# Kernel optimization log

Hardware: AMD Instinct MI355X
Metric: run time of the kernel (lower is better)

The kernel has to match this reference:

```python
import jax, jax.numpy as jnp
import numpy as np

BS, SLEN = 4, 4096
H, ZD, VD = 8, 128, 256
CHUNK = 1024
NEG = -1e9


def _rope(x, cos, sin):
    # x: [B, S, H, D]; cos/sin: [S, D//2] (llama-style complex pair rotation)
    b, s, h, d = x.shape
    xr, xi = x.reshape(b, s, h, d // 2, 2)[..., 0], x.reshape(b, s, h, d // 2, 2)[..., 1]
    c = cos[None, :, None, :]
    sn = sin[None, :, None, :]
    orr = xr * c - xi * sn
    oii = xr * sn + xi * c
    return jnp.stack([orr, oii], axis=-1).reshape(b, s, h, d)


def setup_inputs() -> dict:
    key = jax.random.key(0)
    k1, k2, k3 = jax.random.split(key, 3)
    xq = jax.random.normal(k1, (BS, SLEN, H * ZD), dtype=jnp.float32)
    xk = jax.random.normal(k2, (BS, SLEN, H * ZD), dtype=jnp.float32)
    xv = jax.random.normal(k3, (BS, SLEN, H * VD), dtype=jnp.float32)
    # rotary tables over one chunk
    freqs = 1.0 / (10000.0 ** (np.arange(0, ZD, 2, dtype=np.float32) / ZD))  # [ZD//2]
    t = np.arange(CHUNK, dtype=np.float32)
    ang = np.outer(t, freqs)  # [CHUNK, ZD//2]
    cos = jnp.asarray(np.cos(ang), dtype=jnp.float32)
    sin = jnp.asarray(np.sin(ang), dtype=jnp.float32)
    # additive causal mask within a chunk
    causal = np.tril(np.ones((CHUNK, CHUNK), dtype=bool))
    mask = jnp.asarray(np.where(causal, 0.0, NEG).astype(np.float32))
    return {"xq": xq, "xk": xk, "xv": xv, "mask": mask, "cos": cos, "sin": sin}


def reference(xq, xk, xv, mask, cos, sin):
    bs, slen, _ = xq.shape
    nc = slen // CHUNK
    q = xq.reshape(bs * nc, CHUNK, H, ZD)
    k = xk.reshape(bs * nc, CHUNK, H, ZD)
    v = xv.reshape(bs * nc, CHUNK, H, VD)
    # RoPE applied after chunking (slen > chunk_size path)
    q = _rope(q, cos, sin)
    k = _rope(k, cos, sin)
    # block-local causal attention, no 1/sqrt(d) scaling (faithful to source)
    scores = jnp.einsum("bqhd,bkhd->bhqk", q, k) + mask[None, None, :, :]
    probs = jax.nn.softmax(scores.astype(jnp.float32), axis=-1).astype(q.dtype)
    out = jnp.einsum("bhqk,bkhd->bqhd", probs, v)
    return out.reshape(bs, slen, H * VD)
```

## Files before the change

### kernel.cpp

```cpp
#include <hip/hip_runtime.h>


#define NHEAD 8
#define ZDIM  128
#define VDIM  256
#define CHUNK 1024
#define QTILE 128
#define KT    32
#define NW    4

typedef _Float16 f16x8 __attribute__((ext_vector_type(8)));
typedef _Float16 f16x4 __attribute__((ext_vector_type(4)));
typedef __fp16   h16x2 __attribute__((ext_vector_type(2)));
typedef float    f32x4 __attribute__((ext_vector_type(4)));
typedef unsigned int u32;

#define KSTRIDE 136
#define VSTRIDE 40
#define PSTRIDE 76
#define LOG2E   1.44269504088896f
#define RTHR    11.5415603f

__global__ __launch_bounds__(256, 2)
void attn_fused(const float* __restrict__ xq, const float* __restrict__ xk,
                const float* __restrict__ xv, const float* __restrict__ cosT,
                const float* __restrict__ sinT, float* __restrict__ out)
{
  __shared__ _Float16 Klds[2][KT * KSTRIDE];
  __shared__ _Float16 Vlds[2][VDIM * VSTRIDE];
  __shared__ _Float16 Plds[NW * 32 * PSTRIDE];

  const int b = (int)blockIdx.x;
  const int d = (b & 7) * 64 + (b >> 3);
  const int qpair = d & 3;
  const int ch = d >> 2;
  const int h  = ch & 7;
  const int cb = ch >> 3;

  const int tid  = threadIdx.x;
  const int w    = tid >> 6;
  const int lane = tid & 63;
  const int l15  = lane & 15;
  const int lhi  = lane >> 4;

  const size_t row0 = (size_t)cb * CHUNK;

  const int kr   = tid >> 3;
  const int kc0  = (tid & 7) * 16;
  const int vg   = tid >> 5;
  const int vc0  = (tid & 31) * 8;
  const int vsw  = tid & 3;
  const int kblk = vg >> 1;
  const int inb  = (vg & 1) * 4;

  int buf = 0;

  for (int half = 0; half < 2; ++half) {
    const int qt = half ? qpair : (7 - qpair);

    f16x8 qfrag[2][4];
#pragma unroll
    for (int s = 0; s < 2; ++s) {
      const int qrow = qt * QTILE + w * 32 + s * 16 + l15;
      const float* qp = xq + (row0 + qrow) * (size_t)(NHEAD * ZDIM) + h * ZDIM;
      const float* cq = cosT + qrow * (ZDIM / 2);
      const float* sq = sinT + qrow * (ZDIM / 2);
#pragma unroll
      for (int blk = 0; blk < 4; ++blk) {
        const int d0 = blk * 32 + lhi * 8;
        f32x4 a  = *(const f32x4*)(qp + d0);
        f32x4 bb = *(const f32x4*)(qp + d0 + 4);
        union { h16x2 h2[4]; f16x8 v; } fr;
#pragma unroll
        for (int p = 0; p < 4; ++p) {
          const float cv = cq[(d0 >> 1) + p];
          const float sv = sq[(d0 >> 1) + p];
          const float xr = (p < 2 ? a[2 * p] : bb[2 * p - 4]);
          const float xi = (p < 2 ? a[2 * p + 1] : bb[2 * p - 3]);
          fr.h2[p] = __builtin_amdgcn_cvt_pkrtz(xr * cv - xi * sv, xr * sv + xi * cv);
        }
        qfrag[s][blk] = fr.v;
      }
    }

    const f32x4 zf = {0.f, 0.f, 0.f, 0.f};
    f32x4 acc[2][16];
#pragma unroll
    for (int s = 0; s < 2; ++s)
#pragma unroll
      for (int i = 0; i < 16; ++i) acc[s][i] = zf;
    float mrun2[2][4], lrun[2][4];
#pragma unroll
    for (int s = 0; s < 2; ++s)
#pragma unroll
      for (int r = 0; r < 4; ++r) { mrun2[s][r] = -1e30f; lrun[s][r] = 0.f; }

    const int nkt = 4 * (qt + 1);
    const int wq0 = qt * QTILE + w * 32;

    for (int kt = 0; kt < nkt; ++kt) {
      const int ktb = kt * KT;
      {
        const int krow = ktb + kr;
        const float* kp = xk + (row0 + krow) * (size_t)(NHEAD * ZDIM) + h * ZDIM + kc0;
        const float* ck = cosT + krow * (ZDIM / 2) + (kc0 >> 1);
        const float* sk = sinT + krow * (ZDIM / 2) + (kc0 >> 1);
        f32x4 k0 = *(const f32x4*)(kp);      f32x4 k1 = *(const f32x4*)(kp + 4);
        f32x4 k2 = *(const f32x4*)(kp + 8);  f32x4 k3 = *(const f32x4*)(kp + 12);
        f32x4 c0 = *(const f32x4*)(ck);      f32x4 c1 = *(const f32x4*)(ck + 4);
        f32x4 s0 = *(const f32x4*)(sk);      f32x4 s1 = *(const f32x4*)(sk + 4);
        union { h16x2 h2[8]; u32 u[8]; } ko;
#pragma unroll
        for (int p = 0; p < 8; ++p) {
          const float cv = (p < 4 ? c0[p] : c1[p - 4]);
          const float sv = (p < 4 ? s0[p] : s1[p - 4]);
          const int j = 2 * p;
          const float xr = (j < 4 ? k0[j] : j < 8 ? k1[j - 4] : j < 12 ? k2[j - 8] : k3[j - 12]);
          const float xi = (j + 1 < 4 ? k0[j + 1] : j + 1 < 8 ? k1[j - 3] : j + 1 < 12 ? k2[j - 7] : k3[j - 11]);
          ko.h2[p] = __builtin_amdgcn_cvt_pkrtz(xr * cv - xi * sv, xr * sv + xi * cv);
        }
        u32* kdst = (u32*)&Klds[buf][kr * KSTRIDE + kc0];
        kdst[0] = ko.u[0]; kdst[1] = ko.u[1]; kdst[2] = ko.u[2]; kdst[3] = ko.u[3];
        kdst[4] = ko.u[4]; kdst[5] = ko.u[5]; kdst[6] = ko.u[6]; kdst[7] = ko.u[7];
      }
      {
        const int vrow = ktb + vg * 4;
        const float* vp = xv + (row0 + vrow) * (size_t)(NHEAD * VDIM) + h * VDIM + vc0;
        f32x4 v0 = *(const f32x4*)(vp);         f32x4 v1 = *(const f32x4*)(vp + 4);
        f32x4 v2 = *(const f32x4*)(vp + 2048);  f32x4 v3 = *(const f32x4*)(vp + 2052);
        f32x4 v4 = *(const f32x4*)(vp + 4096);  f32x4 v5 = *(const f32x4*)(vp + 4100);
        f32x4 v6 = *(const f32x4*)(vp + 6144);  f32x4 v7 = *(const f32x4*)(vp + 6148);
#pragma unroll
        for (int ci = 0; ci < 8; ++ci) {
          const float e0 = (ci < 4 ? v0[ci] : v1[ci - 4]);
          const float e1 = (ci < 4 ? v2[ci] : v3[ci - 4]);
          const float e2 = (ci < 4 ? v4[ci] : v5[ci - 4]);
          const float e3 = (ci < 4 ? v6[ci] : v7[ci - 4]);
          union { h16x2 a[2]; f16x4 v; } t;
          t.a[0] = __builtin_amdgcn_cvt_pkrtz(e0, e1);
          t.a[1] = __builtin_amdgcn_cvt_pkrtz(e2, e3);
          *(f16x4*)&Vlds[buf][(vc0 + ci) * VSTRIDE + ((kblk ^ vsw) * 8) + inb] = t.v;
        }
      }
      __syncthreads();

      if (ktb <= wq0 + 31) {
        f32x4 sf[2][2];
#pragma unroll
        for (int s = 0; s < 2; ++s)
#pragma unroll
          for (int n = 0; n < 2; ++n) sf[s][n] = zf;
#pragma unroll
        for (int n = 0; n < 2; ++n) {
#pragma unroll
          for (int blk = 0; blk < 4; ++blk) {
            f16x8 bfr = *(const f16x8*)&Klds[buf][(n * 16 + l15) * KSTRIDE + blk * 32 + lhi * 8];
            sf[0][n] = __builtin_amdgcn_mfma_f32_16x16x32_f16(qfrag[0][blk], bfr, sf[0][n], 0, 0, 0);
            sf[1][n] = __builtin_amdgcn_mfma_f32_16x16x32_f16(qfrag[1][blk], bfr, sf[1][n], 0, 0, 0);
          }
        }

        if (ktb + 31 > wq0) {
#pragma unroll
          for (int s = 0; s < 2; ++s) {
            const int qg = wq0 + s * 16 + lhi * 4;
#pragma unroll
            for (int n = 0; n < 2; ++n) {
              const int kg = ktb + n * 16 + l15;
#pragma unroll
              for (int r = 0; r < 4; ++r)
                if (kg > qg + r) sf[s][n][r] = -1.0e9f;
            }
          }
        }

        float mx2v[2][4];
        bool need = false;
#pragma unroll
        for (int s = 0; s < 2; ++s) {
#pragma unroll
          for (int r = 0; r < 4; ++r) {
            float mx = fmaxf(sf[s][0][r], sf[s][1][r]);
            mx = fmaxf(mx, __shfl_xor(mx, 1));
            mx = fmaxf(mx, __shfl_xor(mx, 2));
            mx = fmaxf(mx, __shfl_xor(mx, 4));
            mx = fmaxf(mx, __shfl_xor(mx, 8));
            mx2v[s][r] = mx * LOG2E;
            need = need || (mx2v[s][r] > mrun2[s][r] + RTHR);
          }
        }
        if (__any(need)) {
#pragma unroll
          for (int s = 0; s < 2; ++s) {
#pragma unroll
            for (int r = 0; r < 4; ++r) {
              const float Mn2 = fmaxf(mrun2[s][r], mx2v[s][r]);
              const float al = exp2f(mrun2[s][r] - Mn2);
              mrun2[s][r] = Mn2;
              lrun[s][r] *= al;
#pragma unroll
              for (int i = 0; i < 16; ++i) acc[s][i][r] *= al;
            }
          }
        }
#pragma unroll
        for (int s = 0; s < 2; ++s) {
#pragma unroll
          for (int r = 0; r < 4; ++r) {
#pragma unroll
            for (int n = 0; n < 2; ++n) {
              const float p = exp2f(fmaf(sf[s][n][r], LOG2E, -mrun2[s][r]));
              lrun[s][r] += p;
              Plds[(w * 32 + s * 16 + lhi * 4 + r) * PSTRIDE + n * 16 + l15] = (_Float16)p;
            }
          }
        }

        f16x8 af0 = *(const f16x8*)&Plds[(w * 32 + l15) * PSTRIDE + lhi * 8];
        f16x8 af1 = *(const f16x8*)&Plds[(w * 32 + 16 + l15) * PSTRIDE + lhi * 8];
#pragma unroll
        for (int i = 0; i < 16; ++i) {
          const int vcol = i * 16 + l15;
          f16x8 bfr = *(const f16x8*)&Vlds[buf][vcol * VSTRIDE + ((lhi ^ ((vcol >> 3) & 3)) * 8)];
          acc[0][i] = __builtin_amdgcn_mfma_f32_16x16x32_f16(af0, bfr, acc[0][i], 0, 0, 0);
          acc[1][i] = __builtin_amdgcn_mfma_f32_16x16x32_f16(af1, bfr, acc[1][i], 0, 0, 0);
        }
      }
      buf ^= 1;
    }

#pragma unroll
    for (int s = 0; s < 2; ++s) {
      float linv[4];
#pragma unroll
      for (int r = 0; r < 4; ++r) {
        float ls = lrun[s][r];
        ls += __shfl_xor(ls, 1);
        ls += __shfl_xor(ls, 2);
        ls += __shfl_xor(ls, 4);
        ls += __shfl_xor(ls, 8);
        linv[r] = 1.0f / ls;
      }
      const size_t obase = (row0 + (size_t)qt * QTILE + w * 32 + s * 16) * (size_t)(NHEAD * VDIM) + h * VDIM;
#pragma unroll
      for (int i = 0; i < 16; ++i) {
#pragma unroll
        for (int r = 0; r < 4; ++r) {
          const int q = lhi * 4 + r;
          out[obase + (size_t)q * (NHEAD * VDIM) + i * 16 + l15] = acc[s][i][r] * linv[r];
        }
      }
    }
    __syncthreads();
  }
}

extern "C" void kernel_launch(void* const* d_in, const int* in_sizes, int n_in,
                              void* d_out, int out_size, void* d_ws, size_t ws_size,
                              hipStream_t stream) {
  const float* xq   = (const float*)d_in[0];
  const float* xk   = (const float*)d_in[1];
  const float* xv   = (const float*)d_in[2];
  const float* cosT = (const float*)d_in[4];
  const float* sinT = (const float*)d_in[5];
  float* out = (float*)d_out;

  dim3 grid(512);
  dim3 block(256);
  attn_fused<<<grid, block, 0, stream>>>(xq, xk, xv, cosT, sinT, out);
}
```

Baseline: 210.8 us.

## Switch attention to 32x32 MFMA with transposed scores and register-resident P

Replaces the 16x16x32 MFMA tiling with 32x32x16 MFMA, computing S^T = K·Q so each lane holds one query column and the softmax max and sum need a single cross-half shuffle. P is repacked into A fragments with lane shuffles rather than staged through LDS, which removes the Plds buffer and its round trip. It also adds an XOR swizzle to the K LDS layout, shrinks the V stride, folds LOG2E into Q during RoPE, and raises wave priority around the MFMA blocks. In exchange it uses more accumulator registers, and the rescale and normalize steps now need per-row shuffles.

```diff
diff --git a/kernel.cpp b/kernel.cpp
--- a/kernel.cpp
+++ b/kernel.cpp
@@ -12,12 +12,12 @@
 typedef _Float16 f16x8 __attribute__((ext_vector_type(8)));
 typedef _Float16 f16x4 __attribute__((ext_vector_type(4)));
 typedef __fp16   h16x2 __attribute__((ext_vector_type(2)));
-typedef float    f32x4 __attribute__((ext_vector_type(4)));
+typedef float    f32x4  __attribute__((ext_vector_type(4)));
+typedef float    f32x16 __attribute__((ext_vector_type(16)));
 typedef unsigned int u32;
 
 #define KSTRIDE 136
-#define VSTRIDE 40
-#define PSTRIDE 76
+#define VSTRIDE 36
 #define LOG2E   1.44269504088896f
 #define RTHR    11.5415603f
 
@@ -28,7 +28,6 @@
 {
   __shared__ _Float16 Klds[2][KT * KSTRIDE];
   __shared__ _Float16 Vlds[2][VDIM * VSTRIDE];
-  __shared__ _Float16 Plds[NW * 32 * PSTRIDE];
 
   const int b = (int)blockIdx.x;
   const int d = (b & 7) * 64 + (b >> 3);
@@ -40,13 +39,16 @@
   const int tid  = threadIdx.x;
   const int w    = tid >> 6;
   const int lane = tid & 63;
-  const int l15  = lane & 15;
-  const int lhi  = lane >> 4;
+  const int l31  = lane & 31;
+  const int hi   = lane >> 5;
+  const int vswz = (l31 >> 3) & 3;
+  const int kswz = lane & 15;
 
   const size_t row0 = (size_t)cb * CHUNK;
 
   const int kr   = tid >> 3;
   const int kc0  = (tid & 7) * 16;
+  const int kch0 = (tid & 7) * 2;
   const int vg   = tid >> 5;
   const int vc0  = (tid & 31) * 8;
   const int vsw  = tid & 3;
@@ -57,46 +59,41 @@
 
   for (int half = 0; half < 2; ++half) {
     const int qt = half ? qpair : (7 - qpair);
-
-    f16x8 qfrag[2][4];
-#pragma unroll
-    for (int s = 0; s < 2; ++s) {
-      const int qrow = qt * QTILE + w * 32 + s * 16 + l15;
-      const float* qp = xq + (row0 + qrow) * (size_t)(NHEAD * ZDIM) + h * ZDIM;
-      const float* cq = cosT + qrow * (ZDIM / 2);
-      const float* sq = sinT + qrow * (ZDIM / 2);
-#pragma unroll
-      for (int blk = 0; blk < 4; ++blk) {
-        const int d0 = blk * 32 + lhi * 8;
+    const int wq0 = qt * QTILE + w * 32;
+    const int qg  = wq0 + l31;
+
+    f16x8 qfrag[8];
+    {
+      const float* qp = xq + (row0 + qg) * (size_t)(NHEAD * ZDIM) + h * ZDIM;
+      const float* cq = cosT + qg * (ZDIM / 2);
+      const float* sq = sinT + qg * (ZDIM / 2);
+#pragma unroll
+      for (int dblk = 0; dblk < 8; ++dblk) {
+        const int d0 = dblk * 16 + hi * 8;
         f32x4 a  = *(const f32x4*)(qp + d0);
-        f32x4 bb = *(const f32x4*)(qp + d0 + 4);
+        f32x4 b2 = *(const f32x4*)(qp + d0 + 4);
+        f32x4 cv = *(const f32x4*)(cq + (d0 >> 1));
+        f32x4 sv = *(const f32x4*)(sq + (d0 >> 1));
         union { h16x2 h2[4]; f16x8 v; } fr;
 #pragma unroll
         for (int p = 0; p < 4; ++p) {
-          const float cv = cq[(d0 >> 1) + p];
-          const float sv = sq[(d0 >> 1) + p];
-          const float xr = (p < 2 ? a[2 * p] : bb[2 * p - 4]);
-          const float xi = (p < 2 ? a[2 * p + 1] : bb[2 * p - 3]);
-          fr.h2[p] = __builtin_amdgcn_cvt_pkrtz(xr * cv - xi * sv, xr * sv + xi * cv);
-        }
-        qfrag[s][blk] = fr.v;
+          const float xr = (p < 2 ? a[2 * p] : b2[2 * p - 4]);
+          const float xi = (p < 2 ? a[2 * p + 1] : b2[2 * p - 3]);
+          fr.h2[p] = __builtin_amdgcn_cvt_pkrtz((xr * cv[p] - xi * sv[p]) * LOG2E,
+                                                (xr * sv[p] + xi * cv[p]) * LOG2E);
+        }
+        qfrag[dblk] = fr.v;
       }
     }
 
-    const f32x4 zf = {0.f, 0.f, 0.f, 0.f};
-    f32x4 acc[2][16];
-#pragma unroll
-    for (int s = 0; s < 2; ++s)
-#pragma unroll
-      for (int i = 0; i < 16; ++i) acc[s][i] = zf;
-    float mrun2[2][4], lrun[2][4];
-#pragma unroll
-    for (int s = 0; s < 2; ++s)
-#pragma unroll
-      for (int r = 0; r < 4; ++r) { mrun2[s][r] = -1e30f; lrun[s][r] = 0.f; }
+    const f32x16 zf = {};
+    f32x16 acc[8];
+#pragma unroll
+    for (int g = 0; g < 8; ++g) acc[g] = zf;
+    float mrun = -1e30f;
+    float lrun = 0.f;
 
     const int nkt = 4 * (qt + 1);
-    const int wq0 = qt * QTILE + w * 32;
 
     for (int kt = 0; kt < nkt; ++kt) {
       const int ktb = kt * KT;
@@ -119,9 +116,11 @@
           const float xi = (j + 1 < 4 ? k0[j + 1] : j + 1 < 8 ? k1[j - 3] : j + 1 < 12 ? k2[j - 7] : k3[j - 11]);
           ko.h2[p] = __builtin_amdgcn_cvt_pkrtz(xr * cv - xi * sv, xr * sv + xi * cv);
         }
-        u32* kdst = (u32*)&Klds[buf][kr * KSTRIDE + kc0];
-        kdst[0] = ko.u[0]; kdst[1] = ko.u[1]; kdst[2] = ko.u[2]; kdst[3] = ko.u[3];
-        kdst[4] = ko.u[4]; kdst[5] = ko.u[5]; kdst[6] = ko.u[6]; kdst[7] = ko.u[7];
+        const int sw = kr & 15;
+        u32* p1 = (u32*)&Klds[buf][kr * KSTRIDE + ((kch0 ^ sw) * 8)];
+        p1[0] = ko.u[0]; p1[1] = ko.u[1]; p1[2] = ko.u[2]; p1[3] = ko.u[3];
+        u32* p2 = (u32*)&Klds[buf][kr * KSTRIDE + (((kch0 + 1) ^ sw) * 8)];
+        p2[0] = ko.u[4]; p2[1] = ko.u[5]; p2[2] = ko.u[6]; p2[3] = ko.u[7];
       }
       {
         const int vrow = ktb + vg * 4;
@@ -136,120 +135,100 @@
           const float e1 = (ci < 4 ? v2[ci] : v3[ci - 4]);
           const float e2 = (ci < 4 ? v4[ci] : v5[ci - 4]);
           const float e3 = (ci < 4 ? v6[ci] : v7[ci - 4]);
-          union { h16x2 a[2]; f16x4 v; } t;
-          t.a[0] = __builtin_amdgcn_cvt_pkrtz(e0, e1);
-          t.a[1] = __builtin_amdgcn_cvt_pkrtz(e2, e3);
+          union { h16x2 a2[2]; f16x4 v; } t;
+          t.a2[0] = __builtin_amdgcn_cvt_pkrtz(e0, e1);
+          t.a2[1] = __builtin_amdgcn_cvt_pkrtz(e2, e3);
           *(f16x4*)&Vlds[buf][(vc0 + ci) * VSTRIDE + ((kblk ^ vsw) * 8) + inb] = t.v;
         }
       }
       __syncthreads();
 
       if (ktb <= wq0 + 31) {
-        f32x4 sf[2][2];
-#pragma unroll
-        for (int s = 0; s < 2; ++s)
-#pragma unroll
-          for (int n = 0; n < 2; ++n) sf[s][n] = zf;
-#pragma unroll
-        for (int n = 0; n < 2; ++n) {
-#pragma unroll
-          for (int blk = 0; blk < 4; ++blk) {
-            f16x8 bfr = *(const f16x8*)&Klds[buf][(n * 16 + l15) * KSTRIDE + blk * 32 + lhi * 8];
-            sf[0][n] = __builtin_amdgcn_mfma_f32_16x16x32_f16(qfrag[0][blk], bfr, sf[0][n], 0, 0, 0);
-            sf[1][n] = __builtin_amdgcn_mfma_f32_16x16x32_f16(qfrag[1][blk], bfr, sf[1][n], 0, 0, 0);
+        f32x16 s = {};
+        __builtin_amdgcn_s_setprio(1);
+#pragma unroll
+        for (int dblk = 0; dblk < 8; ++dblk) {
+          f16x8 kf = *(const f16x8*)&Klds[buf][l31 * KSTRIDE + (((dblk * 2 + hi) ^ kswz) * 8)];
+          s = __builtin_amdgcn_mfma_f32_32x32x16_f16(kf, qfrag[dblk], s, 0, 0, 0);
+        }
+        __builtin_amdgcn_s_setprio(0);
+
+        if (ktb + 31 > wq0) {
+#pragma unroll
+          for (int r = 0; r < 16; ++r) {
+            const int kg = ktb + ((r & 3) + 8 * (r >> 2) + 4 * hi);
+            if (kg > qg) s[r] = -1.0e9f;
           }
         }
 
-        if (ktb + 31 > wq0) {
-#pragma unroll
-          for (int s = 0; s < 2; ++s) {
-            const int qg = wq0 + s * 16 + lhi * 4;
-#pragma unroll
-            for (int n = 0; n < 2; ++n) {
-              const int kg = ktb + n * 16 + l15;
-#pragma unroll
-              for (int r = 0; r < 4; ++r)
-                if (kg > qg + r) sf[s][n][r] = -1.0e9f;
-            }
+        float m = s[0];
+#pragma unroll
+        for (int r = 1; r < 16; ++r) m = fmaxf(m, s[r]);
+        m = fmaxf(m, __shfl_xor(m, 32));
+        const bool need = (m > mrun + RTHR);
+        if (__any(need)) {
+          const float Mn = fmaxf(mrun, m);
+          const float al = exp2f(mrun - Mn);
+          mrun = Mn;
+          lrun *= al;
+#pragma unroll
+          for (int r = 0; r < 16; ++r) {
+            const float alr = __shfl(al, (r & 3) + 8 * (r >> 2) + 4 * hi);
+#pragma unroll
+            for (int g = 0; g < 8; ++g) acc[g][r] *= alr;
           }
         }
-
-        float mx2v[2][4];
-        bool need = false;
-#pragma unroll
-        for (int s = 0; s < 2; ++s) {
-#pragma unroll
-          for (int r = 0; r < 4; ++r) {
-            float mx = fmaxf(sf[s][0][r], sf[s][1][r]);
-            mx = fmaxf(mx, __shfl_xor(mx, 1));
-            mx = fmaxf(mx, __shfl_xor(mx, 2));
-            mx = fmaxf(mx, __shfl_xor(mx, 4));
-            mx = fmaxf(mx, __shfl_xor(mx, 8));
-            mx2v[s][r] = mx * LOG2E;
-            need = need || (mx2v[s][r] > mrun2[s][r] + RTHR);
+        float pr[16];
+        float lsum = 0.f;
+#pragma unroll
+        for (int r = 0; r < 16; ++r) {
+          pr[r] = exp2f(s[r] - mrun);
+          lsum += pr[r];
+        }
+        lrun += lsum;
+
+#pragma unroll
+        for (int kb = 0; kb < 2; ++kb) {
+          union { h16x2 h; u32 u; } A_, B_, C_, D_;
+          A_.h = __builtin_amdgcn_cvt_pkrtz(pr[8 * kb + 0], pr[8 * kb + 1]);
+          B_.h = __builtin_amdgcn_cvt_pkrtz(pr[8 * kb + 2], pr[8 * kb + 3]);
+          C_.h = __builtin_amdgcn_cvt_pkrtz(pr[8 * kb + 4], pr[8 * kb + 5]);
+          D_.h = __builtin_amdgcn_cvt_pkrtz(pr[8 * kb + 6], pr[8 * kb + 7]);
+          const u32 G1 = hi ? A_.u : C_.u;
+          const u32 G2 = hi ? B_.u : D_.u;
+          const u32 G1s = (u32)__shfl_xor((int)G1, 32);
+          const u32 G2s = (u32)__shfl_xor((int)G2, 32);
+          union { u32 u[4]; f16x8 v; } af;
+          af.u[0] = hi ? G1s : A_.u;
+          af.u[1] = hi ? G2s : B_.u;
+          af.u[2] = hi ? C_.u : G1s;
+          af.u[3] = hi ? D_.u : G2s;
+          __builtin_amdgcn_s_setprio(1);
+#pragma unroll
+          for (int g = 0; g < 8; ++g) {
+            const int vcol = g * 32 + l31;
+            const int ck = (((kb * 2 + hi) ^ vswz) * 8);
+            union { f16x4 h4[2]; f16x8 v; } bf;
+            bf.h4[0] = *(const f16x4*)&Vlds[buf][vcol * VSTRIDE + ck];
+            bf.h4[1] = *(const f16x4*)&Vlds[buf][vcol * VSTRIDE + ck + 4];
+            acc[g] = __builtin_amdgcn_mfma_f32_32x32x16_f16(af.v, bf.v, acc[g], 0, 0, 0);
           }
-        }
-        if (__any(need)) {
-#pragma unroll
-          for (int s = 0; s < 2; ++s) {
-#pragma unroll
-            for (int r = 0; r < 4; ++r) {
-              const float Mn2 = fmaxf(mrun2[s][r], mx2v[s][r]);
-              const float al = exp2f(mrun2[s][r] - Mn2);
-              mrun2[s][r] = Mn2;
-              lrun[s][r] *= al;
-#pragma unroll
-              for (int i = 0; i < 16; ++i) acc[s][i][r] *= al;
-            }
-          }
-        }
-#pragma unroll
-        for (int s = 0; s < 2; ++s) {
-#pragma unroll
-          for (int r = 0; r < 4; ++r) {
-#pragma unroll
-            for (int n = 0; n < 2; ++n) {
-              const float p = exp2f(fmaf(sf[s][n][r], LOG2E, -mrun2[s][r]));
-              lrun[s][r] += p;
-              Plds[(w * 32 + s * 16 + lhi * 4 + r) * PSTRIDE + n * 16 + l15] = (_Float16)p;
-            }
-          }
-        }
-
-        f16x8 af0 = *(const f16x8*)&Plds[(w * 32 + l15) * PSTRIDE + lhi * 8];
-        f16x8 af1 = *(const f16x8*)&Plds[(w * 32 + 16 + l15) * PSTRIDE + lhi * 8];
-#pragma unroll
-        for (int i = 0; i < 16; ++i) {
-          const int vcol = i * 16 + l15;
-          f16x8 bfr = *(const f16x8*)&Vlds[buf][vcol * VSTRIDE + ((lhi ^ ((vcol >> 3) & 3)) * 8)];
-          acc[0][i] = __builtin_amdgcn_mfma_f32_16x16x32_f16(af0, bfr, acc[0][i], 0, 0, 0);
-          acc[1][i] = __builtin_amdgcn_mfma_f32_16x16x32_f16(af1, bfr, acc[1][i], 0, 0, 0);
+          __builtin_amdgcn_s_setprio(0);
         }
       }
       buf ^= 1;
     }
 
-#pragma unroll
-    for (int s = 0; s < 2; ++s) {
-      float linv[4];
-#pragma unroll
-      for (int r = 0; r < 4; ++r) {
-        float ls = lrun[s][r];
-        ls += __shfl_xor(ls, 1);
-        ls += __shfl_xor(ls, 2);
-        ls += __shfl_xor(ls, 4);
-        ls += __shfl_xor(ls, 8);
-        linv[r] = 1.0f / ls;
-      }
-      const size_t obase = (row0 + (size_t)qt * QTILE + w * 32 + s * 16) * (size_t)(NHEAD * VDIM) + h * VDIM;
-#pragma unroll
-      for (int i = 0; i < 16; ++i) {
-#pragma unroll
-        for (int r = 0; r < 4; ++r) {
-          const int q = lhi * 4 + r;
-          out[obase + (size_t)q * (NHEAD * VDIM) + i * 16 + l15] = acc[s][i][r] * linv[r];
-        }
-      }
+    const float ls = lrun + __shfl_xor(lrun, 32);
+    const float linv = 1.0f / ls;
+#pragma unroll
+    for (int r = 0; r < 16; ++r) {
+      const int qloc = (r & 3) + 8 * (r >> 2) + 4 * hi;
+      const float lr = __shfl(linv, qloc);
+      const size_t ob = (row0 + wq0 + qloc) * (size_t)(NHEAD * VDIM) + h * VDIM + l31;
+#pragma unroll
+      for (int g = 0; g < 8; ++g)
+        out[ob + g * 32] = acc[g][r] * lr;
     }
     __syncthreads();
   }
```

Measured after the change: 192.0 us. 1.1x faster.
